# Kernel tuning notes

Measured on AMD Instinct MI355X. Metric: run time of the kernel, lower is better.

## Reference

```python
import jax, jax.numpy as jnp
import numpy as np

D_MODEL = 64
LN_EPS = 1e-5


def _conv1d(x, w, b, stride, pad):
    # x: (B, Cin, L), w: (Cout, Cin, K)
    y = jax.lax.conv_general_dilated(x, w, (stride,), [(pad, pad)],
                                     dimension_numbers=('NCH', 'OIH', 'NCH'))
    return y + b[None, :, None]


def _layernorm(x, g, b):
    # normalize over last dim (feature dim), matching nn.LayerNorm(d_model)
    m = jnp.mean(x, axis=-1, keepdims=True)
    v = jnp.var(x, axis=-1, keepdims=True)
    return (x - m) * jax.lax.rsqrt(v + LN_EPS) * g + b


def _pos_embed(L, d):
    pos = jnp.arange(L, dtype=jnp.float32)[:, None]
    div = jnp.exp(jnp.arange(0, d, 2, dtype=jnp.float32) * (-np.log(10000.0) / d))
    pe = jnp.zeros((L, d), jnp.float32)
    pe = pe.at[:, 0::2].set(jnp.sin(pos * div))
    pe = pe.at[:, 1::2].set(jnp.cos(pos * div))
    return pe


def setup_inputs():
    key = jax.random.key(0)
    ks = jax.random.split(key, 20)
    B, L, D = 128, 4096, D_MODEL
    G = D // 4  # 16 convs per kernel-size group (kernels cycle [3,5,7,9])
    inp = {'x': jax.random.normal(ks[0], (B, 1, L), jnp.float32)}
    kernels = [3, 5, 7, 9]
    for i, k in enumerate(kernels):
        fan = float(1.0 / np.sqrt(k))
        inp['tok_w%d' % k] = jax.random.uniform(ks[1 + 2 * i], (G, 1, k), jnp.float32, -fan, fan)
        inp['tok_b%d' % k] = jax.random.uniform(ks[2 + 2 * i], (G,), jnp.float32, -fan, fan)
    fan = float(1.0 / np.sqrt(D * 4))
    for j in range(3):
        inp['c_w%d' % (j + 1)] = jax.random.uniform(ks[10 + 2 * j], (D, D, 4), jnp.float32, -fan, fan)
        inp['c_b%d' % (j + 1)] = jax.random.uniform(ks[11 + 2 * j], (D,), jnp.float32, -fan, fan)
    for j in range(2):
        inp['ln_g%d' % (j + 1)] = jnp.ones((D,), jnp.float32)
        inp['ln_b%d' % (j + 1)] = jnp.zeros((D,), jnp.float32)
    return inp


def reference(x, tok_w3, tok_b3, tok_w5, tok_b5, tok_w7, tok_b7, tok_w9, tok_b9,
              c_w1, c_b1, c_w2, c_b2, c_w3, c_b3, ln_g1, ln_b1, ln_g2, ln_b2):
    B, _, L = x.shape
    D = D_MODEL
    # TokenEmbedding: conv i has kernel [3,5,7,9][i%4]; fuse the d_model 1-channel
    # convs into 4 grouped convs (one per kernel size), then interleave channels.
    outs = [
        _conv1d(x, tok_w3, tok_b3, 1, 1),
        _conv1d(x, tok_w5, tok_b5, 1, 2),
        _conv1d(x, tok_w7, tok_b7, 1, 3),
        _conv1d(x, tok_w9, tok_b9, 1, 4),
    ]  # each (B, D//4, L); group g holds channels i with i % 4 == g, ordered by i // 4
    emb = jnp.stack(outs, axis=2).reshape(B, D, L)  # channel i = (i//4)*4 + (i%4)
    # add sinusoidal positional embedding (dropout is identity in eval mode)
    h = emb + _pos_embed(L, D).T[None]  # (B, D, L)
    # CompressionEmbedding: conv(k=4, s=2, p=1) -> tanh -> LN (over D) chain
    h = jnp.tanh(_conv1d(h, c_w1, c_b1, 2, 1))
    h = _layernorm(h.transpose(0, 2, 1), ln_g1, ln_b1).transpose(0, 2, 1)
    h = jnp.tanh(_conv1d(h, c_w2, c_b2, 2, 1))
    h = _layernorm(h.transpose(0, 2, 1), ln_g2, ln_b2).transpose(0, 2, 1)
    h = jnp.tanh(_conv1d(h, c_w3, c_b3, 2, 1))
    return h.transpose(0, 2, 1)  # (B, L//8, D)
```

## Files before the change

### kernel.cpp

```cpp
#include <hip/hip_runtime.h>
#include <math.h>

#define BATCH 128
#define LN_EPS 1e-5f

typedef short bf16x8 __attribute__((ext_vector_type(8)));
typedef short bf16x4 __attribute__((ext_vector_type(4)));
typedef float f32x4  __attribute__((ext_vector_type(4)));

__device__ __forceinline__ ushort f2bf(float f) {
    return __builtin_bit_cast(ushort, (__bf16)f);
}

__device__ __forceinline__ float fast_tanh(float v) {
    float e = __expf(2.f * v);
    return 1.f - 2.f / (e + 1.f);
}

__global__ __launch_bounds__(256, 2)
void prep_kernel(const float* __restrict__ cw1, const float* __restrict__ cw2,
                 const float* __restrict__ cw3,
                 const float* __restrict__ w3, const float* __restrict__ b3,
                 const float* __restrict__ w5, const float* __restrict__ b5,
                 const float* __restrict__ w7, const float* __restrict__ b7,
                 const float* __restrict__ w9, const float* __restrict__ b9,
                 const float* __restrict__ cb1, const float* __restrict__ cb2,
                 const float* __restrict__ cb3,
                 const float* __restrict__ lg1, const float* __restrict__ lb1,
                 const float* __restrict__ lg2, const float* __restrict__ lb2,
                 ushort* __restrict__ Wm23, ushort* __restrict__ Wm1,
                 float* __restrict__ W0c, float* __restrict__ W3c,
                 float* __restrict__ pe1c,
                 float* __restrict__ cb2t, float* __restrict__ B2k0,
                 float* __restrict__ B2k3,
                 float* __restrict__ cb3t, float* __restrict__ B3k0,
                 float* __restrict__ B3k3) {
    const int tid = threadIdx.x;
    const int bx  = blockIdx.x;
    const int idx = bx * 256 + tid;

    __shared__ float tile[64][132];
    __shared__ float red[4][64][24];
    __shared__ float cbred[64][4];

    {
        int s = idx >> 14, r = idx & 16383;
        int j = r & 7, l15 = (r >> 3) & 15, dt = (r >> 7) & 3;
        int quad = (r >> 9) & 3, k2 = (r >> 11) & 1, kk = (r >> 12) & 3;
        int dout = dt * 16 + l15, din = k2 * 32 + quad * 8 + j;
        const float* cw = (s == 0) ? cw2 : cw3;
        const float* lg = (s == 0) ? lg1 : lg2;
        Wm23[idx] = f2bf(cw[dout * 256 + din * 4 + kk] * lg[din]);
    }

    if (bx == 1 && tid < 128) {
        const int s = tid >> 6, ch = tid & 63;
        const float* cw = (s == 0) ? cw2 : cw3;
        const float* lb = (s == 0) ? lb1 : lb2;
        float full = 0.f, k0 = 0.f, k3 = 0.f;
        for (int din = 0; din < 64; ++din) {
            float bv = lb[din];
            const float* wr = cw + ch * 256 + din * 4;
            k0 = fmaf(wr[0], bv, k0);
            k3 = fmaf(wr[3], bv, k3);
            full = fmaf(wr[0] + wr[1] + wr[2] + wr[3], bv, full);
        }
        if (s == 0) { cb2t[ch] = cb2[ch] + full; B2k0[ch] = k0; B2k3[ch] = k3; }
        else        { cb3t[ch] = cb3[ch] + full; B3k0[ch] = k0; B3k3[ch] = k3; }
    }

    if (bx == 0) {
        const int ch = tid & 63, part = tid >> 6;
        const float* cw1row = cw1 + ch * 256;
        float acc[24];
#pragma unroll
        for (int j = 0; j < 24; ++j) acc[j] = 0.f;
        for (int din = part * 16; din < part * 16 + 16; ++din) {
            int ki = din & 3, g = din >> 2;
            float wl[9];
#pragma unroll
            for (int j = 0; j < 9; ++j) wl[j] = 0.f;
            float bias;
            if (ki == 0)      { for (int j = 0; j < 3; ++j) wl[3 + j] = w3[g * 3 + j]; bias = b3[g]; }
            else if (ki == 1) { for (int j = 0; j < 5; ++j) wl[2 + j] = w5[g * 5 + j]; bias = b5[g]; }
            else if (ki == 2) { for (int j = 0; j < 7; ++j) wl[1 + j] = w7[g * 7 + j]; bias = b7[g]; }
            else              { for (int j = 0; j < 9; ++j) wl[j]     = w9[g * 9 + j]; bias = b9[g]; }
#pragma unroll
            for (int kk = 0; kk < 4; ++kk) {
                float c = cw1row[din * 4 + kk];
                acc[12 + kk] += c * bias;
#pragma unroll
                for (int u = 0; u < 9; ++u) acc[kk + u] += c * wl[u];
            }
            float c0 = cw1row[din * 4 + 0], c3 = cw1row[din * 4 + 3];
#pragma unroll
            for (int u = 0; u < 4; ++u) { acc[16 + u] += c0 * wl[5 + u]; acc[20 + u] += c3 * wl[u]; }
        }
#pragma unroll
        for (int j = 0; j < 24; ++j) red[part][ch][j] = acc[j];
    }

    {
        const int pair = tid & 63, part = tid >> 6;
        const int kk = pair >> 4, chl = pair & 15;
        const int ch = (bx & 3) * 16 + chl;
        float s = 0.f;
        for (int din = part * 16; din < part * 16 + 16; ++din) {
            int ki = din & 3, g = din >> 2;
            float bias = (ki == 0) ? b3[g] : (ki == 1) ? b5[g] : (ki == 2) ? b7[g] : b9[g];
            s += cw1[ch * 256 + din * 4 + kk] * bias;
        }
        cbred[pair][part] = s;
    }

    const int l0 = (bx >> 2) * 64;
    const int pin0 = 2 * l0 - 1;
    for (int i2 = tid; i2 < 64 * 130; i2 += 256) {
        int d = i2 / 130, pp = i2 - d * 130;
        int p = pin0 + pp;
        float v = 0.f;
        if (p >= 0 && p < 4096) {
            float dv = __expf((float)(d & ~1) * -0.14391156831212787f);
            float ang = (float)p * dv;
            v = (d & 1) ? __cosf(ang) : __sinf(ang);
        }
        tile[d][pp] = v;
    }
    __syncthreads();

    if (bx == 0 && tid < 64) {
        const int ch = tid;
        float w24[24];
#pragma unroll
        for (int j = 0; j < 24; ++j)
            w24[j] = red[0][ch][j] + red[1][ch][j] + red[2][ch][j] + red[3][ch][j];
        int dt = ch >> 4, l15 = ch & 15;
#pragma unroll
        for (int quad = 0; quad < 4; ++quad)
#pragma unroll
            for (int j = 0; j < 8; ++j) {
                int k = quad * 8 + j;
                Wm1[((quad * 4 + dt) * 16 + l15) * 8 + j] = f2bf(k < 12 ? w24[k] : 0.f);
            }
#pragma unroll
        for (int u = 0; u < 4; ++u) { W0c[ch * 4 + u] = w24[16 + u]; W3c[ch * 4 + u] = w24[20 + u]; }
    }

    const int lane = tid & 63, wv = tid >> 6;
    const int l = l0 + lane;
    const int chl0 = wv * 4;
    const int db = (bx & 3) * 16 + chl0;
    float a4[4];
#pragma unroll
    for (int j = 0; j < 4; ++j) {
        int chl = chl0 + j;
        float cbk0 = cbred[0 * 16 + chl][0] + cbred[0 * 16 + chl][1] + cbred[0 * 16 + chl][2] + cbred[0 * 16 + chl][3];
        float cbk1 = cbred[1 * 16 + chl][0] + cbred[1 * 16 + chl][1] + cbred[1 * 16 + chl][2] + cbred[1 * 16 + chl][3];
        float cbk2 = cbred[2 * 16 + chl][0] + cbred[2 * 16 + chl][1] + cbred[2 * 16 + chl][2] + cbred[2 * 16 + chl][3];
        float cbk3 = cbred[3 * 16 + chl][0] + cbred[3 * 16 + chl][1] + cbred[3 * 16 + chl][2] + cbred[3 * 16 + chl][3];
        float a = cb1[db + j] + cbk1 + cbk2;
        if (l > 0) a += cbk0;
        if (l < 2047) a += cbk3;
        a4[j] = a;
    }
    for (int din = 0; din < 64; ++din) {
        float v0 = tile[din][2 * lane + 0], v1 = tile[din][2 * lane + 1];
        float v2 = tile[din][2 * lane + 2], v3 = tile[din][2 * lane + 3];
        const float* wb = cw1 + din * 4;
#pragma unroll
        for (int j = 0; j < 4; ++j) {
            const float* wj = wb + (db + j) * 256;
            a4[j] = fmaf(v0, wj[0], fmaf(v1, wj[1], fmaf(v2, wj[2], fmaf(v3, wj[3], a4[j]))));
        }
    }
    *(float4*)(pe1c + (size_t)l * 64 + db) = make_float4(a4[0], a4[1], a4[2], a4[3]);
}

__global__ __launch_bounds__(256, 2)
void mega_kernel(const float* __restrict__ x,
                 const ushort* __restrict__ Wm1, const ushort* __restrict__ Wm23,
                 const float* __restrict__ pe1c,
                 const float* __restrict__ W0c, const float* __restrict__ W3c,
                 const float* __restrict__ cb2t, const float* __restrict__ B2k0,
                 const float* __restrict__ B2k3,
                 const float* __restrict__ cb3t, const float* __restrict__ B3k0,
                 const float* __restrict__ B3k3,
                 float* __restrict__ out) {
    const int b0 = blockIdx.y;
    const int g0 = blockIdx.x * 32;
    const int tid = threadIdx.x;

    __shared__ __align__(16) ushort xs[2][320];
    __shared__ __align__(16) ushort TE1[2][68][72];
    __shared__ __align__(16) ushort TO1[2][68][72];
    __shared__ __align__(16) ushort TE2[2][34][72];
    __shared__ __align__(16) ushort TO2[2][34][72];

    for (int i = tid; i < 640; i += 256) {
        int ba = (i >= 320) ? 1 : 0, j = i - ba * 320;
        int g = 8 * g0 - 11 + j;
        float v = (g >= 0 && g < 4096) ? x[(size_t)(b0 + ba * 64) * 4096 + g] : 0.f;
        xs[ba][j] = f2bf(v);
    }
    __syncthreads();

    const int wv = tid >> 6, lane = tid & 63;
    const int quad = lane >> 4, l15 = lane & 15;

    {
        bf16x8 afr1[4];
#pragma unroll
        for (int dt = 0; dt < 4; ++dt)
            afr1[dt] = *(const bf16x8*)&Wm1[((quad * 4 + dt) * 16 + l15) * 8];
        const int qstart = 4 * g0 - 3;
        for (int pass = wv; pass < 9; pass += 4) {
            const int m = pass * 16 + l15;
            const int q = qstart + m;
            const int qc = (q < 0) ? 0 : ((q > 2047) ? 2047 : q);
            const float* pb_ = pe1c + (size_t)qc * 64 + quad * 4;
            float4 pv[4];
#pragma unroll
            for (int dt = 0; dt < 4; ++dt) pv[dt] = *(const float4*)(pb_ + dt * 16);
            union { bf16x8 v; unsigned u[4]; } tA, tB;
            const unsigned* pA = (const unsigned*)&xs[0][2 * m + 8 * quad];
            const unsigned* pB = (const unsigned*)&xs[1][2 * m + 8 * quad];
#pragma unroll
            for (int i = 0; i < 4; ++i) { tA.u[i] = pA[i]; tB.u[i] = pB[i]; }
            f32x4 a1[2][4];
#pragma unroll
            for (int dt = 0; dt < 4; ++dt) {
                f32x4 c;
                c[0] = pv[dt].x; c[1] = pv[dt].y; c[2] = pv[dt].z; c[3] = pv[dt].w;
                a1[0][dt] = __builtin_amdgcn_mfma_f32_16x16x32_bf16(afr1[dt], tA.v, c, 0, 0, 0);
                a1[1][dt] = __builtin_amdgcn_mfma_f32_16x16x32_bf16(afr1[dt], tB.v, c, 0, 0, 0);
            }
            if (m < 134) {
                if (q >= 0 && q < 2048) {
#pragma unroll
                    for (int ba = 0; ba < 2; ++ba) {
                        ushort* dst = (m & 1) ? &TE1[ba][(m + 1) >> 1][0]
                                              : &TO1[ba][m >> 1][0];
                        if (q == 0 || q == 2047) {
                            const float* Wc = (q == 0) ? W0c : W3c;
                            const float* xe = x + (size_t)(b0 + ba * 64) * 4096
                                                + ((q == 0) ? 0 : 4092);
                            float x0 = xe[0], x1 = xe[1], x2 = xe[2], x3 = xe[3];
#pragma unroll
                            for (int dt = 0; dt < 4; ++dt)
#pragma unroll
                                for (int r = 0; r < 4; ++r) {
                                    const float* wc = Wc + (dt * 16 + quad * 4 + r) * 4;
                                    a1[ba][dt][r] -= wc[0] * x0 + wc[1] * x1 + wc[2] * x2 + wc[3] * x3;
                                }
                        }
                        float v[16], s = 0.f, s2 = 0.f;
#pragma unroll
                        for (int dt = 0; dt < 4; ++dt)
#pragma unroll
                            for (int r = 0; r < 4; ++r) {
                                float t = fast_tanh(a1[ba][dt][r]);
                                v[dt * 4 + r] = t;
                                s += t;
                                s2 = fmaf(t, t, s2);
                            }
                        s += __shfl_xor(s, 16, 64);
                        s += __shfl_xor(s, 32, 64);
                        s2 += __shfl_xor(s2, 16, 64);
                        s2 += __shfl_xor(s2, 32, 64);
                        float mean = s * 0.015625f;
                        float var = fmaf(-mean, mean, s2 * 0.015625f);
                        float rstd = rsqrtf(var + LN_EPS);
                        float nmr = -mean * rstd;
#pragma unroll
                        for (int dt = 0; dt < 4; ++dt) {
                            bf16x4 pk;
#pragma unroll
                            for (int r = 0; r < 4; ++r)
                                pk[r] = (short)f2bf(fmaf(v[dt * 4 + r], rstd, nmr));
                            *(bf16x4*)(dst + dt * 16 + quad * 4) = pk;
                        }
                    }
                } else {
                    bf16x4 z; z[0] = 0; z[1] = 0; z[2] = 0; z[3] = 0;
#pragma unroll
                    for (int ba = 0; ba < 2; ++ba) {
                        ushort* dst = (m & 1) ? &TE1[ba][(m + 1) >> 1][0]
                                              : &TO1[ba][m >> 1][0];
#pragma unroll
                        for (int dt = 0; dt < 4; ++dt)
                            *(bf16x4*)(dst + dt * 16 + quad * 4) = z;
                    }
                }
            }
        }
    }
    __syncthreads();

    {
        f32x4 cfr2[4];
#pragma unroll
        for (int dt = 0; dt < 4; ++dt) {
            float4 cv = *(const float4*)(cb2t + dt * 16 + quad * 4);
            cfr2[dt][0] = cv.x; cfr2[dt][1] = cv.y; cfr2[dt][2] = cv.z; cfr2[dt][3] = cv.w;
        }
        for (int pass = wv; pass < 5; pass += 4) {
            const int n = pass * 16 + l15;
            const int nc = (n < 66) ? n : 65;
            f32x4 a2[2][4];
#pragma unroll
            for (int dt = 0; dt < 4; ++dt) { a2[0][dt] = cfr2[dt]; a2[1][dt] = cfr2[dt]; }
#pragma unroll
            for (int kk = 0; kk < 4; ++kk) {
                const int row = nc + ((kk + 1) >> 1);
#pragma unroll
                for (int k2 = 0; k2 < 2; ++k2) {
                    bf16x8 bfrA = (kk & 1) ? *(const bf16x8*)&TE1[0][row][k2 * 32 + quad * 8]
                                           : *(const bf16x8*)&TO1[0][row][k2 * 32 + quad * 8];
                    bf16x8 bfrB = (kk & 1) ? *(const bf16x8*)&TE1[1][row][k2 * 32 + quad * 8]
                                           : *(const bf16x8*)&TO1[1][row][k2 * 32 + quad * 8];
                    const ushort* wb = Wm23 + ((((kk * 2 + k2) * 4 + quad) * 4) * 16) * 8;
#pragma unroll
                    for (int dt = 0; dt < 4; ++dt) {
                        bf16x8 afr = *(const bf16x8*)(wb + ((size_t)(dt * 16 + l15)) * 8);
                        a2[0][dt] = __builtin_amdgcn_mfma_f32_16x16x32_bf16(afr, bfrA, a2[0][dt], 0, 0, 0);
                        a2[1][dt] = __builtin_amdgcn_mfma_f32_16x16x32_bf16(afr, bfrB, a2[1][dt], 0, 0, 0);
                    }
                }
            }
            if (n < 66) {
                const int p = 2 * g0 - 1 + n;
                if (p >= 0 && p < 1024) {
#pragma unroll
                    for (int ba = 0; ba < 2; ++ba) {
                        ushort* dst = (n & 1) ? &TE2[ba][(n + 1) >> 1][0]
                                              : &TO2[ba][n >> 1][0];
                        if (p == 0 || p == 1023) {
                            const float* Bc = (p == 0) ? B2k0 : B2k3;
#pragma unroll
                            for (int dt = 0; dt < 4; ++dt)
#pragma unroll
                                for (int r = 0; r < 4; ++r)
                                    a2[ba][dt][r] -= Bc[dt * 16 + quad * 4 + r];
                        }
                        float v[16], s = 0.f, s2 = 0.f;
#pragma unroll
                        for (int dt = 0; dt < 4; ++dt)
#pragma unroll
                            for (int r = 0; r < 4; ++r) {
                                float t = fast_tanh(a2[ba][dt][r]);
                                v[dt * 4 + r] = t;
                                s += t;
                                s2 = fmaf(t, t, s2);
                            }
                        s += __shfl_xor(s, 16, 64);
                        s += __shfl_xor(s, 32, 64);
                        s2 += __shfl_xor(s2, 16, 64);
                        s2 += __shfl_xor(s2, 32, 64);
                        float mean = s * 0.015625f;
                        float var = fmaf(-mean, mean, s2 * 0.015625f);
                        float rstd = rsqrtf(var + LN_EPS);
                        float nmr = -mean * rstd;
#pragma unroll
                        for (int dt = 0; dt < 4; ++dt) {
                            bf16x4 pk;
#pragma unroll
                            for (int r = 0; r < 4; ++r)
                                pk[r] = (short)f2bf(fmaf(v[dt * 4 + r], rstd, nmr));
                            *(bf16x4*)(dst + dt * 16 + quad * 4) = pk;
                        }
                    }
                } else {
                    bf16x4 z; z[0] = 0; z[1] = 0; z[2] = 0; z[3] = 0;
#pragma unroll
                    for (int ba = 0; ba < 2; ++ba) {
                        ushort* dst = (n & 1) ? &TE2[ba][(n + 1) >> 1][0]
                                              : &TO2[ba][n >> 1][0];
#pragma unroll
                        for (int dt = 0; dt < 4; ++dt)
                            *(bf16x4*)(dst + dt * 16 + quad * 4) = z;
                    }
                }
            }
        }
    }
    __syncthreads();

    {
        const int m3 = (wv & 1) * 16 + l15;
        const int dth = wv >> 1;
        f32x4 a3[2][2];
#pragma unroll
        for (int d2 = 0; d2 < 2; ++d2) {
            float4 cv = *(const float4*)(cb3t + (dth * 2 + d2) * 16 + quad * 4);
            f32x4 c; c[0] = cv.x; c[1] = cv.y; c[2] = cv.z; c[3] = cv.w;
            a3[0][d2] = c; a3[1][d2] = c;
        }
        const ushort* Wg3 = Wm23 + 16384;
#pragma unroll
        for (int kk = 0; kk < 4; ++kk) {
            const int row = m3 + ((kk + 1) >> 1);
#pragma unroll
            for (int k2 = 0; k2 < 2; ++k2) {
                bf16x8 bfrA = (kk & 1) ? *(const bf16x8*)&TE2[0][row][k2 * 32 + quad * 8]
                                       : *(const bf16x8*)&TO2[0][row][k2 * 32 + quad * 8];
                bf16x8 bfrB = (kk & 1) ? *(const bf16x8*)&TE2[1][row][k2 * 32 + quad * 8]
                                       : *(const bf16x8*)&TO2[1][row][k2 * 32 + quad * 8];
                const ushort* wb = Wg3 + ((((kk * 2 + k2) * 4 + quad) * 4) * 16) * 8;
#pragma unroll
                for (int d2 = 0; d2 < 2; ++d2) {
                    const int dt = dth * 2 + d2;
                    bf16x8 afr = *(const bf16x8*)(wb + ((size_t)(dt * 16 + l15)) * 8);
                    a3[0][d2] = __builtin_amdgcn_mfma_f32_16x16x32_bf16(afr, bfrA, a3[0][d2], 0, 0, 0);
                    a3[1][d2] = __builtin_amdgcn_mfma_f32_16x16x32_bf16(afr, bfrB, a3[1][d2], 0, 0, 0);
                }
            }
        }
        const int l = g0 + m3;
        if (l == 0 || l == 511) {
            const float* Bc = (l == 0) ? B3k0 : B3k3;
#pragma unroll
            for (int ba = 0; ba < 2; ++ba)
#pragma unroll
                for (int d2 = 0; d2 < 2; ++d2)
#pragma unroll
                    for (int r = 0; r < 4; ++r)
                        a3[ba][d2][r] -= Bc[(dth * 2 + d2) * 16 + quad * 4 + r];
        }
#pragma unroll
        for (int ba = 0; ba < 2; ++ba) {
            float* ob = out + ((size_t)((b0 + ba * 64) * 512) + l) * 64;
#pragma unroll
            for (int d2 = 0; d2 < 2; ++d2) {
                const int dt = dth * 2 + d2;
                float4 st = make_float4(fast_tanh(a3[ba][d2][0]),
                                        fast_tanh(a3[ba][d2][1]),
                                        fast_tanh(a3[ba][d2][2]),
                                        fast_tanh(a3[ba][d2][3]));
                *(float4*)(ob + dt * 16 + quad * 4) = st;
            }
        }
    }
}

extern "C" void kernel_launch(void* const* d_in, const int* in_sizes, int n_in,
                              void* d_out, int out_size, void* d_ws, size_t ws_size,
                              hipStream_t stream) {
    (void)in_sizes; (void)n_in; (void)out_size; (void)ws_size;
    const float* x   = (const float*)d_in[0];
    const float* w3  = (const float*)d_in[1];
    const float* b3  = (const float*)d_in[2];
    const float* w5  = (const float*)d_in[3];
    const float* b5  = (const float*)d_in[4];
    const float* w7  = (const float*)d_in[5];
    const float* b7  = (const float*)d_in[6];
    const float* w9  = (const float*)d_in[7];
    const float* b9  = (const float*)d_in[8];
    const float* cw1 = (const float*)d_in[9];
    const float* cb1 = (const float*)d_in[10];
    const float* cw2 = (const float*)d_in[11];
    const float* cb2 = (const float*)d_in[12];
    const float* cw3 = (const float*)d_in[13];
    const float* cb3 = (const float*)d_in[14];
    const float* lg1 = (const float*)d_in[15];
    const float* lb1 = (const float*)d_in[16];
    const float* lg2 = (const float*)d_in[17];
    const float* lb2 = (const float*)d_in[18];
    float* out = (float*)d_out;

    char* w = (char*)d_ws;
    ushort* Wm23 = (ushort*)(w + 0);
    ushort* Wm1  = (ushort*)(w + 65536);
    float*  W0c  = (float*)(w + 69632);
    float*  W3c  = (float*)(w + 70656);
    float*  cb2t = (float*)(w + 71680);
    float*  B2k0 = (float*)(w + 71936);
    float*  B2k3 = (float*)(w + 72192);
    float*  cb3t = (float*)(w + 72448);
    float*  B3k0 = (float*)(w + 72704);
    float*  B3k3 = (float*)(w + 72960);
    float*  pe1c = (float*)(w + 73216);

    prep_kernel<<<128, 256, 0, stream>>>(cw1, cw2, cw3, w3, b3, w5, b5, w7, b7, w9, b9,
                                         cb1, cb2, cb3, lg1, lb1, lg2, lb2,
                                         Wm23, Wm1, W0c, W3c, pe1c,
                                         cb2t, B2k0, B2k3, cb3t, B3k0, B3k3);
    mega_kernel<<<dim3(16, BATCH / 2), 256, 0, stream>>>(
        x, Wm1, Wm23, pe1c, W0c, W3c, cb2t, B2k0, B2k3, cb3t, B3k0, B3k3, out);
}
```

Baseline: 154.9 us.

## Fold token-conv biases into pos-embed tile and spread prep over more blocks

```diff
diff --git a/kernel.cpp b/kernel.cpp
--- a/kernel.cpp
+++ b/kernel.cpp
@@ -37,13 +37,12 @@
                  float* __restrict__ B3k3) {
     const int tid = threadIdx.x;
     const int bx  = blockIdx.x;
-    const int idx = bx * 256 + tid;
-
-    __shared__ float tile[64][132];
+
+    __shared__ float tile[64][12];
     __shared__ float red[4][64][24];
-    __shared__ float cbred[64][4];
-
-    {
+
+    if (tid < 64) {
+        int idx = bx * 64 + tid;
         int s = idx >> 14, r = idx & 16383;
         int j = r & 7, l15 = (r >> 3) & 15, dt = (r >> 7) & 3;
         int quad = (r >> 9) & 3, k2 = (r >> 11) & 1, kk = (r >> 12) & 3;
@@ -80,15 +79,13 @@
             float wl[9];
 #pragma unroll
             for (int j = 0; j < 9; ++j) wl[j] = 0.f;
-            float bias;
-            if (ki == 0)      { for (int j = 0; j < 3; ++j) wl[3 + j] = w3[g * 3 + j]; bias = b3[g]; }
-            else if (ki == 1) { for (int j = 0; j < 5; ++j) wl[2 + j] = w5[g * 5 + j]; bias = b5[g]; }
-            else if (ki == 2) { for (int j = 0; j < 7; ++j) wl[1 + j] = w7[g * 7 + j]; bias = b7[g]; }
-            else              { for (int j = 0; j < 9; ++j) wl[j]     = w9[g * 9 + j]; bias = b9[g]; }
+            if (ki == 0)      { for (int j = 0; j < 3; ++j) wl[3 + j] = w3[g * 3 + j]; }
+            else if (ki == 1) { for (int j = 0; j < 5; ++j) wl[2 + j] = w5[g * 5 + j]; }
+            else if (ki == 2) { for (int j = 0; j < 7; ++j) wl[1 + j] = w7[g * 7 + j]; }
+            else              { for (int j = 0; j < 9; ++j) wl[j]     = w9[g * 9 + j]; }
 #pragma unroll
             for (int kk = 0; kk < 4; ++kk) {
                 float c = cw1row[din * 4 + kk];
-                acc[12 + kk] += c * bias;
 #pragma unroll
                 for (int u = 0; u < 9; ++u) acc[kk + u] += c * wl[u];
             }
@@ -100,31 +97,21 @@
         for (int j = 0; j < 24; ++j) red[part][ch][j] = acc[j];
     }
 
-    {
-        const int pair = tid & 63, part = tid >> 6;
-        const int kk = pair >> 4, chl = pair & 15;
-        const int ch = (bx & 3) * 16 + chl;
-        float s = 0.f;
-        for (int din = part * 16; din < part * 16 + 16; ++din) {
-            int ki = din & 3, g = din >> 2;
-            float bias = (ki == 0) ? b3[g] : (ki == 1) ? b5[g] : (ki == 2) ? b7[g] : b9[g];
-            s += cw1[ch * 256 + din * 4 + kk] * bias;
-        }
-        cbred[pair][part] = s;
-    }
-
-    const int l0 = (bx >> 2) * 64;
-    const int pin0 = 2 * l0 - 1;
-    for (int i2 = tid; i2 < 64 * 130; i2 += 256) {
-        int d = i2 / 130, pp = i2 - d * 130;
-        int p = pin0 + pp;
-        float v = 0.f;
+    for (int i = tid; i < 320; i += 256) {
+        int d2 = i / 10, pp = i - d2 * 10;
+        int p = 8 * bx - 1 + pp;
+        int din0 = 2 * d2, g = d2 >> 1;
+        float sv = 0.f, cv = 0.f;
         if (p >= 0 && p < 4096) {
-            float dv = __expf((float)(d & ~1) * -0.14391156831212787f);
-            float ang = (float)p * dv;
-            v = (d & 1) ? __cosf(ang) : __sinf(ang);
-        }
-        tile[d][pp] = v;
+            float dv = __expf((float)din0 * -0.14391156831212787f);
+            float s, c;
+            __sincosf((float)p * dv, &s, &c);
+            bool lo = (din0 & 3) == 0;
+            sv = s + (lo ? b3[g] : b7[g]);
+            cv = c + (lo ? b5[g] : b9[g]);
+        }
+        tile[din0][pp] = sv;
+        tile[din0 + 1][pp] = cv;
     }
     __syncthreads();
 
@@ -146,34 +133,20 @@
         for (int u = 0; u < 4; ++u) { W0c[ch * 4 + u] = w24[16 + u]; W3c[ch * 4 + u] = w24[20 + u]; }
     }
 
-    const int lane = tid & 63, wv = tid >> 6;
-    const int l = l0 + lane;
-    const int chl0 = wv * 4;
-    const int db = (bx & 3) * 16 + chl0;
-    float a4[4];
-#pragma unroll
-    for (int j = 0; j < 4; ++j) {
-        int chl = chl0 + j;
-        float cbk0 = cbred[0 * 16 + chl][0] + cbred[0 * 16 + chl][1] + cbred[0 * 16 + chl][2] + cbred[0 * 16 + chl][3];
-        float cbk1 = cbred[1 * 16 + chl][0] + cbred[1 * 16 + chl][1] + cbred[1 * 16 + chl][2] + cbred[1 * 16 + chl][3];
-        float cbk2 = cbred[2 * 16 + chl][0] + cbred[2 * 16 + chl][1] + cbred[2 * 16 + chl][2] + cbred[2 * 16 + chl][3];
-        float cbk3 = cbred[3 * 16 + chl][0] + cbred[3 * 16 + chl][1] + cbred[3 * 16 + chl][2] + cbred[3 * 16 + chl][3];
-        float a = cb1[db + j] + cbk1 + cbk2;
-        if (l > 0) a += cbk0;
-        if (l < 2047) a += cbk3;
-        a4[j] = a;
-    }
-    for (int din = 0; din < 64; ++din) {
-        float v0 = tile[din][2 * lane + 0], v1 = tile[din][2 * lane + 1];
-        float v2 = tile[din][2 * lane + 2], v3 = tile[din][2 * lane + 3];
-        const float* wb = cw1 + din * 4;
-#pragma unroll
-        for (int j = 0; j < 4; ++j) {
-            const float* wj = wb + (db + j) * 256;
-            a4[j] = fmaf(v0, wj[0], fmaf(v1, wj[1], fmaf(v2, wj[2], fmaf(v3, wj[3], a4[j]))));
-        }
-    }
-    *(float4*)(pe1c + (size_t)l * 64 + db) = make_float4(a4[0], a4[1], a4[2], a4[3]);
+    {
+        const int ll = tid >> 6, ch = tid & 63;
+        const int l = bx * 4 + ll;
+        float acc = cb1[ch];
+        const float* cwr = cw1 + ch * 256;
+        for (int din = 0; din < 64; ++din) {
+            float4 w = *(const float4*)(cwr + din * 4);
+            acc = fmaf(w.x, tile[din][2 * ll + 0],
+                  fmaf(w.y, tile[din][2 * ll + 1],
+                  fmaf(w.z, tile[din][2 * ll + 2],
+                  fmaf(w.w, tile[din][2 * ll + 3], acc))));
+        }
+        pe1c[(size_t)l * 64 + ch] = acc;
+    }
 }
 
 __global__ __launch_bounds__(256, 2)
@@ -480,7 +453,7 @@
     float*  B3k3 = (float*)(w + 72960);
     float*  pe1c = (float*)(w + 73216);
 
-    prep_kernel<<<128, 256, 0, stream>>>(cw1, cw2, cw3, w3, b3, w5, b5, w7, b7, w9, b9,
+    prep_kernel<<<512, 256, 0, stream>>>(cw1, cw2, cw3, w3, b3, w5, b5, w7, b7, w9, b9,
                                          cb1, cb2, cb3, lg1, lb1, lg2, lb2,
                                          Wm23, Wm1, W0c, W3c, pe1c,
                                          cb2t, B2k0, B2k3, cb3t, B3k0, B3k3);
```

Result: no change. 152.0 us (-1.9%).
